# Optimization experiments

Measured on AMD Instinct MI355X. Metric: run time of the kernel, lower is better.

The kernel has to match this reference:

```python
import jax, jax.numpy as jnp
import numpy as np


def setup_inputs() -> dict:
    key = jax.random.key(0)
    x = jax.random.normal(key, (2, 64, 128), dtype=jnp.float32)
    return {"x": x}


def reference(x):
    # Faithful vectorization of the triple-permutation range-mean loop.
    # Original: for all permutations (lm, tr, sp) of range(L) (all distinct),
    #   dist[:, lm, tr, sp] = concat(mean(x[:, min(lm,sp):max(lm,sp)]),
    #                                 mean(x[:, min(tr,sp):max(tr,sp)]))
    # Non-permutation index triples (any two equal) remain zero.
    B, L, F = x.shape
    # Exclusive prefix sum: P[:, i] = sum_{j < i} x[:, j]  -> O(1) range sums
    P = jnp.concatenate([jnp.zeros((B, 1, F), x.dtype), jnp.cumsum(x, axis=1)], axis=1)  # [B, L+1, F]
    idx = jnp.arange(L)
    lo = jnp.minimum(idx[:, None], idx[None, :])  # [L, L]
    hi = jnp.maximum(idx[:, None], idx[None, :])  # [L, L]
    denom = jnp.maximum(hi - lo, 1).astype(x.dtype)  # avoid 0/0 on diagonal (masked out later)
    # M[b, a, c, f] = mean of x[b, min(a,c):max(a,c), f]
    M = (P[:, hi] - P[:, lo]) / denom[None, :, :, None]  # [B, L, L, F]

    first = jnp.broadcast_to(M[:, :, None, :, :], (B, L, L, L, F))   # indexed by (lm, sp), bcast over tr
    second = jnp.broadcast_to(M[:, None, :, :, :], (B, L, L, L, F))  # indexed by (tr, sp), bcast over lm

    lm = idx[:, None, None]
    tr = idx[None, :, None]
    sp = idx[None, None, :]
    distinct = ((lm != tr) & (lm != sp) & (tr != sp))  # [L, L, L]
    mask = distinct[None, :, :, :, None].astype(x.dtype)

    dist = jnp.concatenate([first, second], axis=-1) * mask  # [B, L, L, L, 2F]
    return dist
```

## Files before the change

kernel.cpp:

```cpp
#include <hip/hip_runtime.h>
#include <hip/hip_bf16.h>


#define B_ 2
#define L_ 64
#define F_ 128

__device__ float g_P[B_ * (L_ + 1) * F_];

__global__ void prefix_kernel(const float* __restrict__ x) {
    const int b = blockIdx.x;
    const int f = threadIdx.x;
    const float* xb = x + b * L_ * F_ + f;
    float* Pb = g_P + b * (L_ + 1) * F_ + f;

    float v[L_];
#pragma unroll
    for (int r = 0; r < L_; ++r) v[r] = xb[r * F_];

    float run = 0.0f;
    Pb[0] = 0.0f;
#pragma unroll
    for (int r = 0; r < L_; ++r) {
        run += v[r];
        Pb[(r + 1) * F_] = run;
    }
}

__global__ __launch_bounds__(256) void writer_kernel(float4* __restrict__ out,
                                                     int total4) {
    const int stride = gridDim.x * blockDim.x;
    for (int idx4 = blockIdx.x * blockDim.x + threadIdx.x; idx4 < total4;
         idx4 += stride) {
        const int f4 = idx4 & 63;
        const int s  = (idx4 >> 6)  & 63;
        const int t  = (idx4 >> 12) & 63;
        const int a  = (idx4 >> 18) & 63;
        const int b  = idx4 >> 24;

        const bool distinct = (a != t) & (a != s) & (t != s);

        float4 v;
        if (!distinct) {
            v = make_float4(0.f, 0.f, 0.f, 0.f);
        } else {
            const int i  = (f4 < 32) ? a : t;
            const int fb = (f4 & 31) << 2;
            const int lo = min(i, s);
            const int hi = max(i, s);
            const int d  = hi - lo;
            const float* base = g_P + ((b * (L_ + 1)) << 7) + fb;
            const float4 phi = *reinterpret_cast<const float4*>(base + (hi << 7));
            const float4 plo = *reinterpret_cast<const float4*>(base + (lo << 7));
            const float r = __builtin_amdgcn_rcpf((float)d);
            v = make_float4((phi.x - plo.x) * r, (phi.y - plo.y) * r,
                            (phi.z - plo.z) * r, (phi.w - plo.w) * r);
        }
        out[idx4] = v;
    }
}

extern "C" void kernel_launch(void* const* d_in, const int* in_sizes, int n_in,
                              void* d_out, int out_size, void* d_ws, size_t ws_size,
                              hipStream_t stream) {
    const float* x = (const float*)d_in[0];
    float4* out = (float4*)d_out;
    const int total4 = out_size / 4;

    prefix_kernel<<<B_, F_, 0, stream>>>(x);
    writer_kernel<<<2048, 256, 0, stream>>>(out, total4);
}
```

Before: 114.5 us.

## Assign one (b,a,t) row per block with nontemporal stores and fast zero path

Replaces the grid-stride writer with one block per (b,a,t) triple. Each thread writes 16 float4 values across the s dimension using nontemporal stores. When a==t the block writes zeros without loading the prefix sums, and the per-element index decoding is simplified. The aim is to cut cache pollution and index arithmetic in a store-bandwidth-bound kernel. It launches far more blocks than before.

```diff
diff --git a/kernel.cpp b/kernel.cpp
--- a/kernel.cpp
+++ b/kernel.cpp
@@ -5,6 +5,8 @@
 #define B_ 2
 #define L_ 64
 #define F_ 128
+
+typedef float f32x4 __attribute__((ext_vector_type(4)));
 
 __device__ float g_P[B_ * (L_ + 1) * F_];
 
@@ -27,36 +29,44 @@
     }
 }
 
-__global__ __launch_bounds__(256) void writer_kernel(float4* __restrict__ out,
-                                                     int total4) {
-    const int stride = gridDim.x * blockDim.x;
-    for (int idx4 = blockIdx.x * blockDim.x + threadIdx.x; idx4 < total4;
-         idx4 += stride) {
-        const int f4 = idx4 & 63;
-        const int s  = (idx4 >> 6)  & 63;
-        const int t  = (idx4 >> 12) & 63;
-        const int a  = (idx4 >> 18) & 63;
-        const int b  = idx4 >> 24;
+__global__ __launch_bounds__(256) void writer_kernel(f32x4* __restrict__ out) {
+    const int bat = blockIdx.x;
+    const int t = bat & 63;
+    const int a = (bat >> 6) & 63;
+    const int b = bat >> 12;
+    const int tid = threadIdx.x;
+    const int f4 = tid & 63;
+    const int sw = tid >> 6;
+    const int s0 = sw << 4;
+    f32x4* o = out + (size_t)bat * 4096 + s0 * 64 + f4;
 
-        const bool distinct = (a != t) & (a != s) & (t != s);
+    const f32x4 z = {0.f, 0.f, 0.f, 0.f};
 
-        float4 v;
-        if (!distinct) {
-            v = make_float4(0.f, 0.f, 0.f, 0.f);
+    if (a == t) {
+#pragma unroll
+        for (int k = 0; k < 16; ++k)
+            __builtin_nontemporal_store(z, o + k * 64);
+        return;
+    }
+
+    const int i = (f4 < 32) ? a : t;
+    const float* base = g_P + ((b * (L_ + 1)) << 7) + ((f4 & 31) << 2);
+
+#pragma unroll
+    for (int k = 0; k < 16; ++k) {
+        const int s = s0 + k;
+        f32x4 v;
+        if (s == a || s == t) {
+            v = z;
         } else {
-            const int i  = (f4 < 32) ? a : t;
-            const int fb = (f4 & 31) << 2;
             const int lo = min(i, s);
             const int hi = max(i, s);
-            const int d  = hi - lo;
-            const float* base = g_P + ((b * (L_ + 1)) << 7) + fb;
-            const float4 phi = *reinterpret_cast<const float4*>(base + (hi << 7));
-            const float4 plo = *reinterpret_cast<const float4*>(base + (lo << 7));
-            const float r = __builtin_amdgcn_rcpf((float)d);
-            v = make_float4((phi.x - plo.x) * r, (phi.y - plo.y) * r,
-                            (phi.z - plo.z) * r, (phi.w - plo.w) * r);
+            const float r = __builtin_amdgcn_rcpf((float)(hi - lo));
+            const f32x4 phi = *reinterpret_cast<const f32x4*>(base + (hi << 7));
+            const f32x4 plo = *reinterpret_cast<const f32x4*>(base + (lo << 7));
+            v = (phi - plo) * r;
         }
-        out[idx4] = v;
+        __builtin_nontemporal_store(v, o + k * 64);
     }
 }
 
@@ -64,9 +74,8 @@
                               void* d_out, int out_size, void* d_ws, size_t ws_size,
                               hipStream_t stream) {
     const float* x = (const float*)d_in[0];
-    float4* out = (float4*)d_out;
-    const int total4 = out_size / 4;
+    f32x4* out = (f32x4*)d_out;
 
     prefix_kernel<<<B_, F_, 0, stream>>>(x);
-    writer_kernel<<<2048, 256, 0, stream>>>(out, total4);
+    writer_kernel<<<B_ * L_ * L_, 256, 0, stream>>>(out);
 }
```

Result: faster. 109.6 us (-4.2%).
